# Kernel optimization log

Measured on AMD Instinct MI355X. Metric: run time of the kernel, lower is better.

## Reference

```python
import jax, jax.numpy as jnp
import numpy as np


def setup_inputs() -> dict:
    key = jax.random.key(0)
    ks = jax.random.split(key, 6)
    b, c, h, w = 8, 256, 48, 48
    return {
        "qry_fts": jax.random.normal(ks[0], (b, c, h, w), dtype=jnp.float32),
        "mask_fts": jax.random.normal(ks[1], (b, c, h, w), dtype=jnp.float32),
        "fts": jax.random.normal(ks[2], (b, c, h, w), dtype=jnp.float32),
        "Wq": jax.random.normal(ks[3], (c, c), dtype=jnp.float32) * (1.0 / np.sqrt(c)),
        "Wk": jax.random.normal(ks[4], (c, c), dtype=jnp.float32) * (1.0 / np.sqrt(c)),
        "Wv": jax.random.normal(ks[5], (c, c), dtype=jnp.float32) * (1.0 / np.sqrt(c)),
        "mu": jnp.full((1,), 0.5, dtype=jnp.float32),
    }


def reference(qry_fts, mask_fts, fts, Wq, Wk, Wv, mu):
    b, c, h, w = qry_fts.shape
    # flatten spatial dims to tokens: [b, N, c], N = h*w
    q_tok = qry_fts.reshape(b, c, h * w).transpose(0, 2, 1)
    m_tok = mask_fts.reshape(b, c, h * w).transpose(0, 2, 1)
    f_tok = fts.reshape(b, c, h * w).transpose(0, 2, 1)

    # torch Linear(no bias): y = x @ W^T with W [out,in]
    Q = jnp.einsum("bnc,dc->bnd", q_tok, Wq)
    K1 = jnp.einsum("bnc,dc->bnd", f_tok, Wk)
    K2 = jnp.einsum("bnc,dc->bnd", m_tok, Wk)
    V = jnp.einsum("bnc,dc->bnd", f_tok, Wv)

    A1 = jax.nn.softmax(jnp.einsum("bqd,bkd->bqk", Q, K1), axis=-1)
    A2 = jax.nn.softmax(jnp.einsum("bqd,bkd->bqk", Q, K2), axis=-1)
    A = (A1 * 0.5 + A2 * mu[0]) / (0.5 + mu[0])

    att = jnp.einsum("bqk,bkd->bqd", A, V)  # [b, N, c]
    att = att.reshape(b, h, w, c).transpose(0, 3, 1, 2)
    return qry_fts + att
```

## Files before the change

kernel.cpp:

```cpp
#include <hip/hip_runtime.h>
#include <math.h>

#define BB 8
#define CC 256
#define NTOK 2304
#define NPL 36
#define LOG2E 1.4426950408889634f
#define BIAS2 72.134752f

typedef __attribute__((ext_vector_type(4))) float f32x4;
typedef __attribute__((ext_vector_type(8))) short s16x8;
typedef __attribute__((ext_vector_type(4))) short s16x4;

__device__ inline unsigned short f2bf(float x) {
  unsigned u = __builtin_bit_cast(unsigned, x);
  return (unsigned short)((u + 0x7FFFu + ((u >> 16) & 1u)) >> 16);
}
__device__ inline float bf2f(unsigned short h) {
  return __builtin_bit_cast(float, (unsigned)h << 16);
}
__device__ inline unsigned short f2h(float x) {
  _Float16 h = (_Float16)x;
  return __builtin_bit_cast(unsigned short, h);
}

__device__ inline void async16(void* lds, const void* g) {
  __builtin_amdgcn_global_load_lds(
      (const __attribute__((address_space(1))) unsigned int*)g,
      (__attribute__((address_space(3))) unsigned int*)lds, 16, 0, 0);
}

__global__ __launch_bounds__(256)
void prep_kernel(const float* __restrict__ X, unsigned short* __restrict__ Xt) {
  __shared__ float Ls[64][65];
  const int t = threadIdx.x;
  const int n0 = blockIdx.x * 64, c0 = blockIdx.y * 64, b = blockIdx.z;
  const float* Xb = X + (size_t)b * CC * NTOK;
  unsigned short* Yb = Xt + (size_t)b * CC * NTOK;

  #pragma unroll
  for (int rr = 0; rr < 16; rr++) {
    int cl = rr * 4 + (t >> 6);
    Ls[cl][t & 63] = Xb[(size_t)(c0 + cl) * NTOK + n0 + (t & 63)];
  }
  __syncthreads();
  #pragma unroll
  for (int rr = 0; rr < 8; rr++) {
    int nl = rr * 8 + (t >> 5);
    int cl = (t & 31) * 2;
    unsigned v = (unsigned)f2h(Ls[cl][nl]) | ((unsigned)f2h(Ls[cl + 1][nl]) << 16);
    *(unsigned*)((char*)Yb + ((size_t)(n0 + nl) * CC + c0 + cl) * 2) = v;
  }
}

__global__ __launch_bounds__(256)
void wconv_kernel(const float* __restrict__ Wq, const float* __restrict__ Wk,
                  const float* __restrict__ Wv, unsigned short* __restrict__ Wqh,
                  unsigned short* __restrict__ Wkh, unsigned short* __restrict__ Wvh) {
  const float* src = (blockIdx.y == 0) ? Wq : (blockIdx.y == 1) ? Wk : Wv;
  unsigned short* dst = (blockIdx.y == 0) ? Wqh : (blockIdx.y == 1) ? Wkh : Wvh;
  int gi = (blockIdx.x * 256 + threadIdx.x) * 4;
  f32x4 v = *(const f32x4*)(src + gi);
  s16x4 o;
  #pragma unroll
  for (int i = 0; i < 4; i++) o[i] = (short)f2h(v[i]);
  *(s16x4*)(dst + gi) = o;
}

template<int MODE>
__global__ __launch_bounds__(256, 2)
void gemm_kernel(const unsigned short* __restrict__ Xt, const unsigned short* __restrict__ Wh,
                 unsigned short* __restrict__ Y) {
  __shared__ alignas(16) char smem[32768];

  const int t = threadIdx.x;
  const int w = t >> 6, l = t & 63, g = l >> 4, c = l & 15;
  const int bid = blockIdx.x;
  const int b = bid & 7, nt = bid >> 3;
  const int n0w = nt * 64 + w * 16;
  const size_t bo = (size_t)b * CC * NTOK;

  const char* Xb = (const char*)(Xt + bo);
  const char* Wb = (const char*)Wh;
  char* Yb = (char*)(Y + bo);

  int koff[4], cdst[4];
  #pragma unroll
  for (int j = 0; j < 4; j++) {
    int ck = w + 4 * j;
    int row = ck * 2 + (l >> 5);
    koff[j] = row * 512 + (((l & 31) * 16) ^ ((row & 7) << 4));
    cdst[j] = ck * 1024 + l * 16;
  }
  int kxor[8];
  #pragma unroll
  for (int dc = 0; dc < 8; dc++)
    kxor[dc] = (dc * 64 + g * 16) ^ ((c & 7) << 4);

  s16x8 xa[8];
  #pragma unroll
  for (int dc = 0; dc < 8; dc++)
    xa[dc] = *(const s16x8*)(Xb + (n0w + c) * 512 + dc * 64 + g * 16);

  f32x4 acc[16];

#define STAGE_W(WB, TILE)                                            \
  do {                                                               \
    _Pragma("unroll")                                                \
    for (int j_ = 0; j_ < 4; j_++)                                   \
      async16((WB) + cdst[j_], Wb + (TILE) * 16384 + koff[j_]);      \
  } while (0)

  STAGE_W(smem, 0);
  __syncthreads();

  #pragma unroll
  for (int ph = 0; ph < 8; ph++) {
    char* cur = smem + (ph & 1) * 16384;
    if (ph < 7) STAGE_W(smem + ((ph & 1) ^ 1) * 16384, ph + 1);
    __builtin_amdgcn_s_setprio(1);
    #pragma unroll
    for (int s = 0; s < 2; s++) {
      const char* Kt = cur + (s * 16 + c) * 512;
      f32x4 sa = (f32x4){0.f, 0.f, 0.f, 0.f};
      #pragma unroll
      for (int dc = 0; dc < 8; dc++) {
        s16x8 wf = *(const s16x8*)(Kt + kxor[dc]);
        sa = __builtin_amdgcn_mfma_f32_16x16x32_f16(xa[dc], wf, sa, 0, 0, 0);
      }
      acc[ph * 2 + s] = sa;
    }
    __builtin_amdgcn_s_setprio(0);
    __syncthreads();
  }
#undef STAGE_W

  if (MODE == 0 || MODE == 1) {
    unsigned short* Ws = (unsigned short*)(smem + w * 8192);
    #pragma unroll
    for (int dt = 0; dt < 16; dt++)
      #pragma unroll
      for (int j = 0; j < 4; j++) {
        float v = (MODE == 0) ? acc[dt][j] * LOG2E : acc[dt][j];
        Ws[(g * 4 + j) * 256 + dt * 16 + c] = f2h(v);
      }
    #pragma unroll
    for (int r = 0; r < 16; r++) {
      s16x4 v = *(const s16x4*)&Ws[r * 256 + l * 4];
      *(s16x4*)(Yb + (size_t)(n0w + r) * 512 + l * 8) = v;
    }
  } else {
    unsigned short* Vs = (unsigned short*)(smem + w * 8192);
    #pragma unroll
    for (int dt = 0; dt < 16; dt++) {
      s16x4 pv;
      #pragma unroll
      for (int j = 0; j < 4; j++) pv[j] = (short)f2bf(acc[dt][j]);
      *(s16x4*)&Vs[c * 20 + g * 4] = pv;
      s16x4 vv = *(const s16x4*)&Vs[(l >> 2) * 20 + (l & 3) * 4];
      *(s16x4*)(Yb + (size_t)(dt * 16 + (l >> 2)) * 4608 + (size_t)(n0w + (l & 3) * 4) * 2) = vv;
    }
  }
}

__global__ __launch_bounds__(256, 2)
void attn_kernel(const unsigned short* __restrict__ Qf, const unsigned short* __restrict__ K1,
                 const unsigned short* __restrict__ K2, const unsigned short* __restrict__ Vt,
                 unsigned short* __restrict__ pa1, unsigned short* __restrict__ pa2,
                 float* __restrict__ lb) {
  __shared__ alignas(16) char smem[79360];
  char* const kb0 = smem;
  char* const kb1 = smem + 16384;

  const int t = threadIdx.x;
  const int w = t >> 6, l = t & 63, g = l >> 4, c = l & 15;
  const int bid = blockIdx.x;
  const int b = bid & 7;
  const int r0 = bid >> 3;
  const int qt = r0 % 36, half = r0 / 36;
  const int q0 = qt * 64 + w * 16;
  const size_t bo = (size_t)b * CC * NTOK;

  const char* Qb  = (const char*)(Qf + bo);
  const char* K1b = (const char*)(K1 + bo);
  const char* K2b = (const char*)(K2 + bo);
  const char* Vtb = (const char*)(Vt + bo);

  float* const Pe0 = (float*)(smem + 65536 + w * 3456);
  float* const Pe1 = Pe0 + 288;
  float* const Pod = Pe0 + 576;

  int koff[2], voff[2], cdst[2];
  #pragma unroll
  for (int j = 0; j < 2; j++) {
    int ck = w + 4 * j;
    int tok = ck * 2 + (l >> 5);
    koff[j] = tok * 512 + (((l & 31) * 16) ^ ((tok & 7) << 4));
    voff[j] = (ck * 32 + (l >> 1)) * 4608 + (((l & 1) ^ ((l >> 3) & 1)) << 4);
    cdst[j] = ck * 1024 + l * 16;
  }

  int kxor[8];
  #pragma unroll
  for (int dc = 0; dc < 8; dc++)
    kxor[dc] = (dc * 64 + g * 16) ^ ((c & 7) << 4);

  s16x8 qf[8];
  #pragma unroll
  for (int dc = 0; dc < 8; dc++)
    qf[dc] = *(const s16x8*)(Qb + (q0 + c) * 512 + dc * 64 + g * 16);

  f32x4 a1[16], a2[16];
  #pragma unroll
  for (int dt = 0; dt < 16; dt++) {
    a1[dt] = (f32x4){0.f, 0.f, 0.f, 0.f};
    a2[dt] = (f32x4){0.f, 0.f, 0.f, 0.f};
  }
  float lr1[4] = {0.f, 0.f, 0.f, 0.f};
  float lr2[4] = {0.f, 0.f, 0.f, 0.f};

#define STAGE_K(KB, TILE)                                                  \
  do {                                                                     \
    _Pragma("unroll")                                                      \
    for (int pp_ = 0; pp_ < 2; pp_++) {                                    \
      const char* ks_ = (pp_ ? K2b : K1b) + (size_t)(TILE) * 8192;         \
      async16((KB) + pp_ * 8192 + cdst[0], ks_ + koff[0]);                 \
      async16((KB) + pp_ * 8192 + cdst[1], ks_ + koff[1]);                 \
    }                                                                      \
  } while (0)

#define STAGE_V(VB, PAIR)                                                  \
  do {                                                                     \
    _Pragma("unroll")                                                      \
    for (int h_ = 0; h_ < 2; h_++) {                                       \
      const char* vs_ = Vtb + (PAIR) * 64 + h_ * 32;                       \
      async16((VB) + h_ * 8192 + cdst[0], vs_ + voff[0]);                  \
      async16((VB) + h_ * 8192 + cdst[1], vs_ + voff[1]);                  \
    }                                                                      \
  } while (0)

  const int tb = half * 72;
  const int pb = half * 36;

  STAGE_K(kb0, tb);
  STAGE_V(smem + 32768, pb);
  __syncthreads();

  for (int p = 0; p < NPL; p++) {
    char* vcur = smem + 32768 + (p & 1) * 16384;
    char* vnxt = smem + 32768 + ((p & 1) ^ 1) * 16384;

    STAGE_K(kb1, tb + 2 * p + 1);
    #pragma unroll
    for (int pp = 0; pp < 2; pp++) {
      const char* Kt = kb0 + pp * 8192 + c * 512;
      f32x4 s = (f32x4){0.f, 0.f, 0.f, 0.f};
      __builtin_amdgcn_s_setprio(1);
      #pragma unroll
      for (int dc = 0; dc < 8; dc++) {
        s16x8 kf = *(const s16x8*)(Kt + kxor[dc]);
        s = __builtin_amdgcn_mfma_f32_16x16x32_f16(qf[dc], kf, s, 0, 0, 0);
      }
      __builtin_amdgcn_s_setprio(0);
      float* lr = pp ? lr2 : lr1;
      float* Pe = pp ? Pe1 : Pe0;
      #pragma unroll
      for (int j = 0; j < 4; j++) {
        float pv = exp2f(s[j] - BIAS2);
        lr[j] += pv;
        Pe[(g * 4 + j) * 18 + c] = pv;
      }
    }
    __syncthreads();

    if (p + 1 < NPL) {
      STAGE_K(kb0, tb + 2 * p + 2);
      STAGE_V(vnxt, pb + p + 1);
    }
    s16x8 pa0, pa1r;
    #pragma unroll
    for (int pp = 0; pp < 2; pp++) {
      const char* Kt = kb1 + pp * 8192 + c * 512;
      f32x4 s = (f32x4){0.f, 0.f, 0.f, 0.f};
      __builtin_amdgcn_s_setprio(1);
      #pragma unroll
      for (int dc = 0; dc < 8; dc++) {
        s16x8 kf = *(const s16x8*)(Kt + kxor[dc]);
        s = __builtin_amdgcn_mfma_f32_16x16x32_f16(qf[dc], kf, s, 0, 0, 0);
      }
      __builtin_amdgcn_s_setprio(0);
      float* lr = pp ? lr2 : lr1;
      #pragma unroll
      for (int j = 0; j < 4; j++) {
        float pv = exp2f(s[j] - BIAS2);
        lr[j] += pv;
        Pod[(g * 4 + j) * 18 + c] = pv;
      }
      const float* src = ((g < 2) ? (pp ? Pe1 : Pe0) : Pod) + c * 18 + (g & 1) * 8;
      s16x8 v;
      #pragma unroll
      for (int i = 0; i < 8; i++) v[i] = (short)f2bf(src[i]);
      if (pp == 0) pa0 = v; else pa1r = v;
    }
    {
      const char* vbase = vcur + ((g >= 2) ? 8192 : 0) + c * 32 +
                          ((((g & 1) ^ ((c >> 2) & 1))) << 4);
      __builtin_amdgcn_s_setprio(1);
      #pragma unroll
      for (int dt = 0; dt < 16; dt++) {
        s16x8 vf = *(const s16x8*)(vbase + dt * 512);
        a1[dt] = __builtin_amdgcn_mfma_f32_16x16x32_bf16(pa0, vf, a1[dt], 0, 0, 0);
        a2[dt] = __builtin_amdgcn_mfma_f32_16x16x32_bf16(pa1r, vf, a2[dt], 0, 0, 0);
      }
      __builtin_amdgcn_s_setprio(0);
    }
    __syncthreads();
  }
#undef STAGE_K
#undef STAGE_V

  #pragma unroll
  for (int j = 0; j < 4; j++) {
    #pragma unroll
    for (int off = 1; off < 16; off <<= 1) {
      lr1[j] += __shfl_xor(lr1[j], off);
      lr2[j] += __shfl_xor(lr2[j], off);
    }
  }
  const int pqidx = (half * 8 + b) * 36 + qt;
  if (c == 0) {
    #pragma unroll
    for (int j = 0; j < 4; j++) {
      int row = w * 16 + g * 4 + j;
      lb[pqidx * 64 + row] = lr1[j];
      lb[36864 + pqidx * 64 + row] = lr2[j];
    }
  }

  unsigned short* const pb1 = pa1 + (size_t)pqidx * 16384;
  unsigned short* const pb2 = pa2 + (size_t)pqidx * 16384;
  float* Ws = (float*)(smem + w * 4352);
  const int q = l & 15, ds = l >> 4;
  #pragma unroll
  for (int ch = 0; ch < 4; ch++) {
    #pragma unroll
    for (int pth = 0; pth < 2; pth++) {
      const f32x4* ap = pth ? a2 : a1;
      unsigned short* pdst = pth ? pb2 : pb1;
      #pragma unroll
      for (int dtp = 0; dtp < 4; dtp++) {
        const int dt = ch * 4 + dtp;
        #pragma unroll
        for (int j = 0; j < 4; j++)
          Ws[(g * 4 + j) * 68 + dtp * 16 + c] = ap[dt][j];
      }
      #pragma unroll
      for (int i = 0; i < 16; i++) {
        int d = ch * 64 + i * 4 + ds;
        pdst[d * 64 + w * 16 + q] = f2bf(Ws[q * 68 + i * 4 + ds]);
      }
      __builtin_amdgcn_s_barrier();
    }
  }
}

__global__ __launch_bounds__(256)
void combine_kernel(const unsigned short* __restrict__ pa1, const unsigned short* __restrict__ pa2,
                    const float* __restrict__ lb, const float* __restrict__ qry,
                    const float* __restrict__ mup, float* __restrict__ out) {
  const int bid = blockIdx.x;
  const int b = bid & 7, qt = bid >> 3;
  const int t = threadIdx.x;
  const int q = t & 63, dr = t >> 6;
  const size_t bo = (size_t)b * CC * NTOK;
  const int q0 = qt * 64;

  const int i0 = (0 * 8 + b) * 36 + qt;
  const int i1 = (1 * 8 + b) * 36 + qt;
  float l1 = lb[i0 * 64 + q] + lb[i1 * 64 + q];
  float l2 = lb[36864 + i0 * 64 + q] + lb[36864 + i1 * 64 + q];
  const float mu = mup[0];
  const float w1 = 0.5f / (0.5f + mu) / l1;
  const float w2 = mu / (0.5f + mu) / l2;

  const unsigned short* p10 = pa1 + (size_t)i0 * 16384;
  const unsigned short* p11 = pa1 + (size_t)i1 * 16384;
  const unsigned short* p20 = pa2 + (size_t)i0 * 16384;
  const unsigned short* p21 = pa2 + (size_t)i1 * 16384;

  #pragma unroll
  for (int i = 0; i < 64; i++) {
    int d = dr * 64 + i;
    int off = d * 64 + q;
    float av1 = bf2f(p10[off]) + bf2f(p11[off]);
    float av2 = bf2f(p20[off]) + bf2f(p21[off]);
    size_t gi = bo + (size_t)d * NTOK + q0 + q;
    out[gi] = qry[gi] + av1 * w1 + av2 * w2;
  }
}

extern "C" void kernel_launch(void* const* d_in, const int* in_sizes, int n_in,
                              void* d_out, int out_size, void* d_ws, size_t ws_size,
                              hipStream_t stream) {
  const float* qry  = (const float*)d_in[0];
  const float* mask = (const float*)d_in[1];
  const float* fts  = (const float*)d_in[2];
  const float* Wq   = (const float*)d_in[3];
  const float* Wk   = (const float*)d_in[4];
  const float* Wv   = (const float*)d_in[5];
  const float* mu   = (const float*)d_in[6];
  float* out = (float*)d_out;

  const size_t SZ = (size_t)BB * CC * NTOK;
  unsigned short* base = (unsigned short*)d_ws;
  unsigned short* PA1 = base;
  unsigned short* PA2 = base + 9437184;
  float*          LB  = (float*)(base + 18874368);
  unsigned short* Xtq = base;
  unsigned short* Xtm = base + SZ;
  unsigned short* Xtf = base + 2 * SZ;
  unsigned short* Qw  = base + 19169280;
  unsigned short* K1w = Qw + SZ;
  unsigned short* K2w = Qw + 2 * SZ;
  unsigned short* Vtw = Qw + 3 * SZ;
  unsigned short* Wqh = Qw + 4 * SZ;
  unsigned short* Wkh = Wqh + CC * CC;
  unsigned short* Wvh = Wkh + CC * CC;

  dim3 pg(NTOK / 64, CC / 64, BB);
  prep_kernel<<<pg, 256, 0, stream>>>(qry,  Xtq);
  prep_kernel<<<pg, 256, 0, stream>>>(mask, Xtm);
  prep_kernel<<<pg, 256, 0, stream>>>(fts,  Xtf);
  wconv_kernel<<<dim3(64, 3), 256, 0, stream>>>(Wq, Wk, Wv, Wqh, Wkh, Wvh);

  const int GG = BB * (NTOK / 64);
  gemm_kernel<0><<<GG, 256, 0, stream>>>(Xtq, Wqh, Qw);
  gemm_kernel<1><<<GG, 256, 0, stream>>>(Xtf, Wkh, K1w);
  gemm_kernel<1><<<GG, 256, 0, stream>>>(Xtm, Wkh, K2w);
  gemm_kernel<2><<<GG, 256, 0, stream>>>(Xtf, Wvh, Vtw);

  attn_kernel<<<2 * GG, 256, 0, stream>>>(Qw, K1w, K2w, Vtw, PA1, PA2, LB);
  combine_kernel<<<GG, 256, 0, stream>>>(PA1, PA2, LB, qry, mu, out);
}
```

Before: 258.6 us.

## Merge prep launches, split MFMA accumulator chains, store attention probs as bf16

The three input-transpose launches become one launch that picks its source and destination from blockIdx.z. In the gemm and attention score loops, the dependent MFMA chain is split into two independent accumulators that are summed at the end, which shortens the serial dependency. The attention kernel now writes the exp probabilities to LDS already converted to bf16 and reads them back with a single 16-byte vector load instead of eight float loads plus conversions. This shrinks the LDS footprint and the conversion work, at the cost of an extra vector add per tile and a slightly different rounding order.

```diff
diff --git a/kernel.cpp b/kernel.cpp
--- a/kernel.cpp
+++ b/kernel.cpp
@@ -31,12 +31,17 @@
 }
 
 __global__ __launch_bounds__(256)
-void prep_kernel(const float* __restrict__ X, unsigned short* __restrict__ Xt) {
+void prep_kernel(const float* __restrict__ X0, const float* __restrict__ X1,
+                 const float* __restrict__ X2, unsigned short* __restrict__ Y0,
+                 unsigned short* __restrict__ Y1, unsigned short* __restrict__ Y2) {
   __shared__ float Ls[64][65];
   const int t = threadIdx.x;
-  const int n0 = blockIdx.x * 64, c0 = blockIdx.y * 64, b = blockIdx.z;
+  const int n0 = blockIdx.x * 64, c0 = blockIdx.y * 64;
+  const int z = blockIdx.z, src = z >> 3, b = z & 7;
+  const float* X = (src == 0) ? X0 : (src == 1) ? X1 : X2;
+  unsigned short* Y = (src == 0) ? Y0 : (src == 1) ? Y1 : Y2;
   const float* Xb = X + (size_t)b * CC * NTOK;
-  unsigned short* Yb = Xt + (size_t)b * CC * NTOK;
+  unsigned short* Yb = Y + (size_t)b * CC * NTOK;
 
   #pragma unroll
   for (int rr = 0; rr < 16; rr++) {
@@ -122,13 +127,13 @@
     #pragma unroll
     for (int s = 0; s < 2; s++) {
       const char* Kt = cur + (s * 16 + c) * 512;
-      f32x4 sa = (f32x4){0.f, 0.f, 0.f, 0.f};
+      f32x4 sx[2] = {(f32x4){0.f, 0.f, 0.f, 0.f}, (f32x4){0.f, 0.f, 0.f, 0.f}};
       #pragma unroll
       for (int dc = 0; dc < 8; dc++) {
         s16x8 wf = *(const s16x8*)(Kt + kxor[dc]);
-        sa = __builtin_amdgcn_mfma_f32_16x16x32_f16(xa[dc], wf, sa, 0, 0, 0);
-      }
-      acc[ph * 2 + s] = sa;
+        sx[dc >> 2] = __builtin_amdgcn_mfma_f32_16x16x32_f16(xa[dc], wf, sx[dc >> 2], 0, 0, 0);
+      }
+      acc[ph * 2 + s] = sx[0] + sx[1];
     }
     __builtin_amdgcn_s_setprio(0);
     __syncthreads();
@@ -168,7 +173,7 @@
                  const unsigned short* __restrict__ K2, const unsigned short* __restrict__ Vt,
                  unsigned short* __restrict__ pa1, unsigned short* __restrict__ pa2,
                  float* __restrict__ lb) {
-  __shared__ alignas(16) char smem[79360];
+  __shared__ alignas(16) char smem[74752];
   char* const kb0 = smem;
   char* const kb1 = smem + 16384;
 
@@ -186,9 +191,9 @@
   const char* K2b = (const char*)(K2 + bo);
   const char* Vtb = (const char*)(Vt + bo);
 
-  float* const Pe0 = (float*)(smem + 65536 + w * 3456);
-  float* const Pe1 = Pe0 + 288;
-  float* const Pod = Pe0 + 576;
+  unsigned short* const Pe0 = (unsigned short*)(smem + 65536 + w * 2304);
+  unsigned short* const Pe1 = Pe0 + 384;
+  unsigned short* const Pod = Pe0 + 768;
 
   int koff[2], voff[2], cdst[2];
   #pragma unroll
@@ -254,21 +259,22 @@
     #pragma unroll
     for (int pp = 0; pp < 2; pp++) {
       const char* Kt = kb0 + pp * 8192 + c * 512;
-      f32x4 s = (f32x4){0.f, 0.f, 0.f, 0.f};
+      f32x4 sx[2] = {(f32x4){0.f, 0.f, 0.f, 0.f}, (f32x4){0.f, 0.f, 0.f, 0.f}};
       __builtin_amdgcn_s_setprio(1);
       #pragma unroll
       for (int dc = 0; dc < 8; dc++) {
         s16x8 kf = *(const s16x8*)(Kt + kxor[dc]);
-        s = __builtin_amdgcn_mfma_f32_16x16x32_f16(qf[dc], kf, s, 0, 0, 0);
+        sx[dc >> 2] = __builtin_amdgcn_mfma_f32_16x16x32_f16(qf[dc], kf, sx[dc >> 2], 0, 0, 0);
       }
       __builtin_amdgcn_s_setprio(0);
+      f32x4 s = sx[0] + sx[1];
       float* lr = pp ? lr2 : lr1;
-      float* Pe = pp ? Pe1 : Pe0;
+      unsigned short* Pe = pp ? Pe1 : Pe0;
       #pragma unroll
       for (int j = 0; j < 4; j++) {
         float pv = exp2f(s[j] - BIAS2);
         lr[j] += pv;
-        Pe[(g * 4 + j) * 18 + c] = pv;
+        Pe[(g * 4 + j) * 24 + c] = f2bf(pv);
       }
     }
     __syncthreads();
@@ -281,25 +287,24 @@
     #pragma unroll
     for (int pp = 0; pp < 2; pp++) {
       const char* Kt = kb1 + pp * 8192 + c * 512;
-      f32x4 s = (f32x4){0.f, 0.f, 0.f, 0.f};
+      f32x4 sx[2] = {(f32x4){0.f, 0.f, 0.f, 0.f}, (f32x4){0.f, 0.f, 0.f, 0.f}};
       __builtin_amdgcn_s_setprio(1);
       #pragma unroll
       for (int dc = 0; dc < 8; dc++) {
         s16x8 kf = *(const s16x8*)(Kt + kxor[dc]);
-        s = __builtin_amdgcn_mfma_f32_16x16x32_f16(qf[dc], kf, s, 0, 0, 0);
+        sx[dc >> 2] = __builtin_amdgcn_mfma_f32_16x16x32_f16(qf[dc], kf, sx[dc >> 2], 0, 0, 0);
       }
       __builtin_amdgcn_s_setprio(0);
+      f32x4 s = sx[0] + sx[1];
       float* lr = pp ? lr2 : lr1;
       #pragma unroll
       for (int j = 0; j < 4; j++) {
         float pv = exp2f(s[j] - BIAS2);
         lr[j] += pv;
-        Pod[(g * 4 + j) * 18 + c] = pv;
-      }
-      const float* src = ((g < 2) ? (pp ? Pe1 : Pe0) : Pod) + c * 18 + (g & 1) * 8;
-      s16x8 v;
-      #pragma unroll
-      for (int i = 0; i < 8; i++) v[i] = (short)f2bf(src[i]);
+        Pod[(g * 4 + j) * 24 + c] = f2bf(pv);
+      }
+      const unsigned short* src = ((g < 2) ? (pp ? Pe1 : Pe0) : Pod) + c * 24 + (g & 1) * 8;
+      s16x8 v = *(const s16x8*)src;
       if (pp == 0) pa0 = v; else pa1r = v;
     }
     {
@@ -427,10 +432,7 @@
   unsigned short* Wkh = Wqh + CC * CC;
   unsigned short* Wvh = Wkh + CC * CC;
 
-  dim3 pg(NTOK / 64, CC / 64, BB);
-  prep_kernel<<<pg, 256, 0, stream>>>(qry,  Xtq);
-  prep_kernel<<<pg, 256, 0, stream>>>(mask, Xtm);
-  prep_kernel<<<pg, 256, 0, stream>>>(fts,  Xtf);
+  prep_kernel<<<dim3(NTOK / 64, CC / 64, 24), 256, 0, stream>>>(qry, mask, fts, Xtq, Xtm, Xtf);
   wconv_kernel<<<dim3(64, 3), 256, 0, stream>>>(Wq, Wk, Wv, Wqh, Wkh, Wvh);
 
   const int GG = BB * (NTOK / 64);
```

After: 247.1 us. 4.5% less time.
